# Kernel tuning notes

Measured on AMD Instinct MI355X. Metric: run time of the kernel, lower is better.

## Reference

```python
import jax, jax.numpy as jnp
import numpy as np

N_HEADS = 16
HEAD_DIM = 64
N_EMBD = 1024
B, S = 2, 2048


def setup_inputs() -> dict:
    key = jax.random.key(0)
    k1, k2, k3 = jax.random.split(key, 3)
    x = jax.random.normal(k1, (B, S, N_EMBD), dtype=jnp.float32)
    W_attn = jax.random.normal(k2, (N_EMBD, 3 * N_EMBD), dtype=jnp.float32) * 0.02
    b_attn = jnp.zeros((3 * N_EMBD,), dtype=jnp.float32)
    W_proj = jax.random.normal(k3, (N_EMBD, N_EMBD), dtype=jnp.float32) * 0.02
    b_proj = jnp.zeros((N_EMBD,), dtype=jnp.float32)
    return {"x": x, "W_attn": W_attn, "b_attn": b_attn, "W_proj": W_proj, "b_proj": b_proj}


def reference(x, W_attn, b_attn, W_proj, b_proj):
    b, s, _ = x.shape
    qkv = x @ W_attn + b_attn  # (b, s, 3*n_embd)
    q, k, v = jnp.split(qkv, 3, axis=-1)
    # (b, s, n_embd) -> (b, h, s, d)
    def heads(t):
        return t.reshape(b, s, N_HEADS, HEAD_DIM).transpose(0, 2, 1, 3)
    q, k, v = heads(q), heads(k), heads(v)
    scale = 1.0 / jnp.sqrt(jnp.float32(HEAD_DIM))
    scores = jnp.einsum("bhqd,bhkd->bhqk", q, k) * scale
    causal = jnp.triu(jnp.full((s, s), -jnp.inf, dtype=scores.dtype), k=1)
    scores = scores + causal[None, None, :, :]
    attn = jax.nn.softmax(scores, axis=-1)
    out = jnp.einsum("bhqk,bhkd->bhqd", attn, v)  # (b, h, s, d)
    out = out.transpose(0, 2, 1, 3).reshape(b, s, N_EMBD)
    return out @ W_proj + b_proj
```

## Files before the change

kernel.cpp:

```cpp
#include <hip/hip_runtime.h>
#include <hip/hip_bf16.h>
#include <stdint.h>
#include <stddef.h>

typedef __bf16 bf16_t;
typedef __attribute__((ext_vector_type(8))) __bf16 bf16x8;
typedef __attribute__((ext_vector_type(4))) __bf16 bf16x4;
typedef __attribute__((ext_vector_type(4))) float f32x4;

#define MFMA_BF16(a, b, c) __builtin_amdgcn_mfma_f32_16x16x32_bf16((a), (b), (c), 0, 0, 0)

__global__ void detect_dtype(const unsigned short* __restrict__ x, int* __restrict__ flag) {
  __shared__ int cnt;
  if (threadIdx.x == 0) cnt = 0;
  __syncthreads();
  int local = 0;
  for (int i = threadIdx.x; i < 16384; i += 256) {
    const int e = (x[i] >> 7) & 0xFF;
    if (e >= 0x8D) local++;
  }
  atomicAdd(&cnt, local);
  __syncthreads();
  if (threadIdx.x == 0) *flag = (cnt > 16) ? 1 : 0;
}

__global__ void cvt_x(const float* __restrict__ in, bf16_t* __restrict__ out,
                      const int* __restrict__ flagp) {
  if (!*flagp) return;
  const size_t i = ((size_t)blockIdx.x * 256 + threadIdx.x) * 8;
  const float4 a = *(const float4*)(in + i), b = *(const float4*)(in + i + 4);
  bf16x8 r;
  r[0] = (__bf16)a.x; r[1] = (__bf16)a.y; r[2] = (__bf16)a.z; r[3] = (__bf16)a.w;
  r[4] = (__bf16)b.x; r[5] = (__bf16)b.y; r[6] = (__bf16)b.z; r[7] = (__bf16)b.w;
  *(bf16x8*)(out + i) = r;
}

__global__ void transpose_any(const void* __restrict__ in, bf16_t* __restrict__ out,
                              int R, int C, const int* __restrict__ flagp) {
  const int isF32 = *flagp;
  __shared__ bf16_t tile[32][33];
  const int tx = threadIdx.x, ty = threadIdx.y;
  const int r0 = blockIdx.y * 32, c0 = blockIdx.x * 32;
#pragma unroll
  for (int i = 0; i < 4; ++i) {
    const size_t idx = (size_t)(r0 + ty + i * 8) * C + (c0 + tx);
    tile[ty + i * 8][tx] = isF32 ? (bf16_t)((const float*)in)[idx]
                                 : ((const bf16_t*)in)[idx];
  }
  __syncthreads();
#pragma unroll
  for (int i = 0; i < 4; ++i)
    out[(size_t)(c0 + ty + i * 8) * R + (r0 + tx)] = tile[tx][ty + i * 8];
}

#define GP 72
template <int MODE>
__global__ __launch_bounds__(256) void gemm_bt(const void* A0,
                        const bf16_t* __restrict__ xb,
                        const bf16_t* __restrict__ Bt,
                        const void* __restrict__ bias,
                        void* C,
                        bf16_t* __restrict__ Qs,
                        bf16_t* __restrict__ Kb,
                        bf16_t* __restrict__ dout_bf,
                        int M, int N, int K,
                        const int* __restrict__ flagp) {
  const int isF32 = *flagp;
  const bf16_t* A = (MODE == 1 && isF32) ? xb : (const bf16_t*)A0;
  bf16_t* Vt = dout_bf + (isF32 ? (size_t)4194304 : 0);

  __shared__ __align__(16) unsigned char pool[128 * GP * 2 * 2];
  bf16_t* As = (bf16_t*)pool;
  bf16_t* Bs = (bf16_t*)pool + 128 * GP;

  const int tid = threadIdx.x;
  const int w = tid >> 6, lane = tid & 63;
  const int quad = lane >> 4, l16 = lane & 15;
  const int wm = w >> 1, wn = w & 1;
  const int m0 = blockIdx.y * 128, n0 = blockIdx.x * 128;

  auto loadA = [&](int k0, int it) -> bf16x8 {
    const int g = it * 256 + tid;
    const int row = g >> 3, col = (g & 7) * 8;
    const int m = m0 + row;
    if (MODE == 2) {
      const size_t aoff =
          ((size_t)((m >> 11) * 16 + (k0 >> 6)) * 2048 + (m & 2047)) * 64 + col;
      return *(const bf16x8*)(A + aoff);
    }
    return *(const bf16x8*)(A + (size_t)m * K + (k0 + col));
  };
  auto loadB = [&](int k0, int it) -> bf16x8 {
    const int g = it * 256 + tid;
    const int row = g >> 3, col = (g & 7) * 8;
    return *(const bf16x8*)(Bt + (size_t)(n0 + row) * K + (k0 + col));
  };

  f32x4 acc[4][4];
#pragma unroll
  for (int i = 0; i < 4; ++i)
#pragma unroll
    for (int j = 0; j < 4; ++j) acc[i][j] = f32x4{0.f, 0.f, 0.f, 0.f};

  auto stage = [&](bf16x8* va, bf16x8* vb) {
#pragma unroll
    for (int it = 0; it < 4; ++it) {
      const int g = it * 256 + tid;
      const int row = g >> 3, col = (g & 7) * 8;
      *(bf16x8*)&As[row * GP + col] = va[it];
      *(bf16x8*)&Bs[row * GP + col] = vb[it];
    }
  };
  auto compute = [&]() {
#pragma unroll
    for (int kc = 0; kc < 2; ++kc) {
      bf16x8 af[4], bfr[4];
#pragma unroll
      for (int i = 0; i < 4; ++i)
        af[i] = *(const bf16x8*)&As[(wm * 64 + i * 16 + l16) * GP + kc * 32 + quad * 8];
#pragma unroll
      for (int j = 0; j < 4; ++j)
        bfr[j] = *(const bf16x8*)&Bs[(wn * 64 + j * 16 + l16) * GP + kc * 32 + quad * 8];
      __builtin_amdgcn_s_setprio(1);
#pragma unroll
      for (int i = 0; i < 4; ++i)
#pragma unroll
        for (int j = 0; j < 4; ++j) acc[i][j] = MFMA_BF16(af[i], bfr[j], acc[i][j]);
      __builtin_amdgcn_s_setprio(0);
    }
  };

  bf16x8 va0[4], vb0[4], va1[4], vb1[4];
#pragma unroll
  for (int it = 0; it < 4; ++it) { va0[it] = loadA(0, it);  vb0[it] = loadB(0, it); }
#pragma unroll
  for (int it = 0; it < 4; ++it) { va1[it] = loadA(64, it); vb1[it] = loadB(64, it); }

  for (int k0 = 0; k0 < K; k0 += 128) {
    __syncthreads();
    stage(va0, vb0);
    __syncthreads();
    if (k0 + 128 < K) {
#pragma unroll
      for (int it = 0; it < 4; ++it) { va0[it] = loadA(k0 + 128, it); vb0[it] = loadB(k0 + 128, it); }
    }
    compute();
    __syncthreads();
    stage(va1, vb1);
    __syncthreads();
    if (k0 + 192 < K) {
#pragma unroll
      for (int it = 0; it < 4; ++it) { va1[it] = loadA(k0 + 192, it); vb1[it] = loadB(k0 + 192, it); }
    }
    compute();
  }

  if (MODE == 1 && n0 >= 2048) {
    bf16_t* tp = (bf16_t*)pool;
    __syncthreads();
#pragma unroll
    for (int j = 0; j < 4; ++j) {
      const int n_l = wn * 64 + j * 16 + l16;
      const int n = n0 + n_l;
      const float bj = isF32 ? ((const float*)bias)[n] : (float)((const bf16_t*)bias)[n];
#pragma unroll
      for (int i = 0; i < 4; ++i) {
#pragma unroll
        for (int r = 0; r < 4; ++r) {
          const int m_l = wm * 64 + i * 16 + quad * 4 + r;
          tp[n_l * 136 + m_l] = (bf16_t)(acc[i][j][r] + bj);
        }
      }
    }
    __syncthreads();
    const int b = m0 >> 11, s0 = m0 & 2047;
#pragma unroll
    for (int seg = 0; seg < 8; ++seg) {
      const int idx = seg * 256 + tid;
      const int n_l = idx >> 4, ms = (idx & 15) * 8;
      const bf16x8 v8 = *(const bf16x8*)&tp[n_l * 136 + ms];
      const int e = (n0 + n_l) & 1023, h = e >> 6, d = e & 63;
      *(bf16x8*)(Vt + ((size_t)(b * 16 + h) * 64 + d) * 2048 + s0 + ms) = v8;
    }
    return;
  }

  if (MODE == 1) {
    bf16_t* tp = (bf16_t*)pool;
    __syncthreads();
    const bool isQ = (n0 < 1024);
    const float sc = isQ ? 0.18033688011f : 1.0f;
#pragma unroll
    for (int j = 0; j < 4; ++j) {
      const int n_l = wn * 64 + j * 16 + l16;
      const int n = n0 + n_l;
      const float bj = isF32 ? ((const float*)bias)[n] : (float)((const bf16_t*)bias)[n];
#pragma unroll
      for (int i = 0; i < 4; ++i) {
#pragma unroll
        for (int r = 0; r < 4; ++r) {
          const int m_l = wm * 64 + i * 16 + quad * 4 + r;
          tp[m_l * 136 + n_l] = (bf16_t)((acc[i][j][r] + bj) * sc);
        }
      }
    }
    __syncthreads();
    bf16_t* dst = isQ ? Qs : Kb;
#pragma unroll
    for (int seg = 0; seg < 8; ++seg) {
      const int idx = seg * 256 + tid;
      const int m_l = idx >> 4, ns = (idx & 15) * 8;
      const bf16x8 v8 = *(const bf16x8*)&tp[m_l * 136 + ns];
      const int m = m0 + m_l;
      const int e = (n0 + ns) & 1023, h = e >> 6, d = e & 63;
      const int bb = m >> 11, s = m & 2047;
      *(bf16x8*)(dst + (((size_t)(bb * 16 + h) * 2048 + s) * 64 + d)) = v8;
    }
    return;
  }

#pragma unroll
  for (int j = 0; j < 4; ++j) {
    const int n = n0 + wn * 64 + j * 16 + l16;
    const float bj = isF32 ? ((const float*)bias)[n] : (float)((const bf16_t*)bias)[n];
#pragma unroll
    for (int i = 0; i < 4; ++i) {
      const int mbase = m0 + wm * 64 + i * 16 + quad * 4;
#pragma unroll
      for (int r = 0; r < 4; ++r) {
        const int m = mbase + r;
        const float v = acc[i][j][r] + bj;
        if (isF32) ((float*)C)[(size_t)m * N + n] = v;
        else       ((bf16_t*)C)[(size_t)m * N + n] = (bf16_t)v;
      }
    }
  }
}

#define AP 72
#define PSP 72
__global__ __launch_bounds__(256, 5) void attn_kernel(bf16_t* QO,
                                                      const bf16_t* __restrict__ Kb,
                                                      const bf16_t* __restrict__ dout_bf,
                                                      const int* __restrict__ flagp) {
  const int isF32 = *flagp;
  const bf16_t* Vt = dout_bf + (isF32 ? (size_t)4194304 : 0);

  __shared__ __align__(16) bf16_t Ks[64 * AP];
  __shared__ __align__(16) bf16_t Vs[64 * AP];
  __shared__ __align__(16) bf16_t Ps[4][16 * PSP];

  const int bid = blockIdx.x;
  const int g = bid >> 5, bh = bid & 31;
  const int qt = (g < 16) ? (31 - g) : (g - 16);

  const int tid = threadIdx.x, w = tid >> 6, lane = tid & 63;
  const int quad = lane >> 4, l16 = lane & 15;

  bf16_t* Q = QO + (size_t)bh * 2048 * 64;
  const bf16_t* K = Kb + (size_t)bh * 2048 * 64;
  const bf16_t* V = Vt + (size_t)bh * 64 * 2048;

  const int qrow = qt * 64 + w * 16;
  const int nkt = qt + 1;

  bf16x8 qf[2];
#pragma unroll
  for (int kk = 0; kk < 2; ++kk)
    qf[kk] = *(const bf16x8*)(Q + (size_t)(qrow + l16) * 64 + kk * 32 + quad * 8);

  f32x4 oacc[4];
  float lsum = 0.f;
#pragma unroll
  for (int jd = 0; jd < 4; ++jd) oacc[jd] = f32x4{0.f, 0.f, 0.f, 0.f};

  const int srow8 = lane >> 3;
  const int scol8 = (lane & 7) * 8;

  auto loadK = [&](int kt, int it) -> bf16x8 {
    const int row = (w + it * 4) * 8 + srow8;
    return *(const bf16x8*)(K + (size_t)(kt * 64 + row) * 64 + scol8);
  };
  auto loadV = [&](int kt, int it) -> bf16x8 {
    const int row = (w + it * 4) * 8 + srow8;
    return *(const bf16x8*)(V + (size_t)row * 2048 + kt * 64 + scol8);
  };

  bf16x8 kv[2], vv[2];
#pragma unroll
  for (int it = 0; it < 2; ++it) { kv[it] = loadK(0, it); vv[it] = loadV(0, it); }

  for (int kt = 0; kt < nkt; ++kt) {
    __syncthreads();
#pragma unroll
    for (int it = 0; it < 2; ++it) {
      const int row = (w + it * 4) * 8 + srow8;
      *(bf16x8*)&Ks[row * AP + scol8] = kv[it];
      *(bf16x8*)&Vs[row * AP + scol8] = vv[it];
    }
    __syncthreads();

    if (kt + 1 < nkt) {
#pragma unroll
      for (int it = 0; it < 2; ++it) { kv[it] = loadK(kt + 1, it); vv[it] = loadV(kt + 1, it); }
    }

    const int kbase = kt * 64;
    f32x4 s[4];
    __builtin_amdgcn_s_setprio(1);
#pragma unroll
    for (int j = 0; j < 4; ++j) {
      const bf16x8 kf0 = *(const bf16x8*)&Ks[(j * 16 + l16) * AP + quad * 8];
      const bf16x8 kf1 = *(const bf16x8*)&Ks[(j * 16 + l16) * AP + 32 + quad * 8];
      f32x4 z = f32x4{0.f, 0.f, 0.f, 0.f};
      z = MFMA_BF16(kf0, qf[0], z);
      s[j] = MFMA_BF16(kf1, qf[1], z);
    }
    __builtin_amdgcn_s_setprio(0);

    if (kbase + 63 > qrow) {
      const int qg = qrow + l16;
#pragma unroll
      for (int j = 0; j < 4; ++j) {
        const int key = kbase + j * 16 + quad * 4;
#pragma unroll
        for (int r = 0; r < 4; ++r)
          if (key + r > qg) s[j][r] = -1e30f;
      }
    }

#pragma unroll
    for (int j = 0; j < 4; ++j) {
      bf16x4 pk;
#pragma unroll
      for (int r = 0; r < 4; ++r) {
        const float p = exp2f(s[j][r]);
        lsum += p;
        pk[r] = (__bf16)p;
      }
      *(bf16x4*)&Ps[w][l16 * PSP + j * 16 + quad * 4] = pk;
    }

    __builtin_amdgcn_s_setprio(1);
#pragma unroll
    for (int kk = 0; kk < 2; ++kk) {
      const bf16x8 pf = *(const bf16x8*)&Ps[w][l16 * PSP + kk * 32 + quad * 8];
#pragma unroll
      for (int jd = 0; jd < 4; ++jd) {
        const bf16x8 vf = *(const bf16x8*)&Vs[(jd * 16 + l16) * AP + kk * 32 + quad * 8];
        oacc[jd] = MFMA_BF16(pf, vf, oacc[jd]);
      }
    }
    __builtin_amdgcn_s_setprio(0);
  }

  lsum += __shfl_xor(lsum, 16);
  lsum += __shfl_xor(lsum, 32);

#pragma unroll
  for (int r = 0; r < 4; ++r) {
    const float lr = fmaxf(__shfl(lsum, quad * 4 + r, 16), 1e-30f);
    const int q = qrow + quad * 4 + r;
#pragma unroll
    for (int jd = 0; jd < 4; ++jd) {
      const int d = jd * 16 + l16;
      Q[(size_t)q * 64 + d] = (bf16_t)(oacc[jd][r] / lr);
    }
  }
}

extern "C" void kernel_launch(void* const* d_in, const int* in_sizes, int n_in,
                              void* d_out, int out_size, void* d_ws, size_t ws_size,
                              hipStream_t stream) {
  const void* x      = d_in[0];
  const void* W_attn = d_in[1];
  const void* b_attn = d_in[2];
  const void* W_proj = d_in[3];
  const void* b_proj = d_in[4];

  char* ws = (char*)d_ws;
  size_t off = 0;
  auto alloc = [&](size_t bytes) {
    char* p = ws + off;
    off += (bytes + 255) & ~(size_t)255;
    return p;
  };
  int*    flag = (int*)alloc(256);
  bf16_t* Qs   = (bf16_t*)alloc((size_t)32 * 2048 * 64 * 2);
  bf16_t* Kb   = (bf16_t*)alloc((size_t)32 * 2048 * 64 * 2);
  bf16_t* Wat  = (bf16_t*)alloc((size_t)3072 * 1024 * 2);
  bf16_t* Wpt  = (bf16_t*)alloc((size_t)1024 * 1024 * 2);
  bf16_t* dout_bf = (bf16_t*)d_out;

  detect_dtype<<<1, 256, 0, stream>>>((const unsigned short*)x, flag);

  cvt_x<<<2048, 256, 0, stream>>>((const float*)x, dout_bf, flag);

  transpose_any<<<dim3(3072 / 32, 1024 / 32), dim3(32, 8), 0, stream>>>(W_attn, Wat, 1024, 3072, flag);
  transpose_any<<<dim3(1024 / 32, 1024 / 32), dim3(32, 8), 0, stream>>>(W_proj, Wpt, 1024, 1024, flag);

  gemm_bt<1><<<dim3(3072 / 128, 4096 / 128), 256, 0, stream>>>(
      x, dout_bf, Wat, b_attn, nullptr, Qs, Kb, dout_bf, 4096, 3072, 1024, flag);

  attn_kernel<<<dim3(1024), 256, 0, stream>>>(Qs, Kb, dout_bf, flag);

  gemm_bt<2><<<dim3(1024 / 128, 4096 / 128), 256, 0, stream>>>(
      Qs, nullptr, Wpt, b_proj, d_out, nullptr, nullptr, dout_bf, 4096, 1024, 1024, flag);
}
```

Baseline: 199.5 us.

## Fuse prep kernels into one launch, single-buffer GEMM loop, drop setprio

Merges dtype detection, x conversion and both weight transposes into one prep kernel, where every block redoes a smaller dtype check on the first 4096 halfwords, which saves three launches. The GEMM main loop goes from two register-prefetch buffers over 128-wide K steps to a single buffer over 64-wide steps, which cuts register pressure but adds a barrier pair per step. The s_setprio hints are removed from both the GEMM and the attention kernels. The detection threshold changes, and each block repeating the check adds a little redundant work.

```diff
diff --git a/kernel.cpp b/kernel.cpp
--- a/kernel.cpp
+++ b/kernel.cpp
@@ -10,42 +10,66 @@
 
 #define MFMA_BF16(a, b, c) __builtin_amdgcn_mfma_f32_16x16x32_bf16((a), (b), (c), 0, 0, 0)
 
-__global__ void detect_dtype(const unsigned short* __restrict__ x, int* __restrict__ flag) {
-  __shared__ int cnt;
-  if (threadIdx.x == 0) cnt = 0;
+__global__ __launch_bounds__(256) void prep(const void* __restrict__ x,
+                                            const void* __restrict__ Wa,
+                                            const void* __restrict__ Wp,
+                                            bf16_t* __restrict__ xb,
+                                            bf16_t* __restrict__ Wat,
+                                            bf16_t* __restrict__ Wpt,
+                                            int* __restrict__ flag) {
+  __shared__ int dcnt;
+  __shared__ bf16_t tile[32][33];
+
+  const int tid = threadIdx.x;
+  if (tid == 0) dcnt = 0;
   __syncthreads();
-  int local = 0;
-  for (int i = threadIdx.x; i < 16384; i += 256) {
-    const int e = (x[i] >> 7) & 0xFF;
-    if (e >= 0x8D) local++;
-  }
-  atomicAdd(&cnt, local);
+  {
+    const unsigned short* p = (const unsigned short*)x + tid * 16;
+    int local = 0;
+#pragma unroll
+    for (int i = 0; i < 16; ++i) {
+      const int e = (p[i] >> 7) & 0xFF;
+      if (e >= 0x8D) local++;
+    }
+    if (local) atomicAdd(&dcnt, local);
+  }
   __syncthreads();
-  if (threadIdx.x == 0) *flag = (cnt > 16) ? 1 : 0;
-}
-
-__global__ void cvt_x(const float* __restrict__ in, bf16_t* __restrict__ out,
-                      const int* __restrict__ flagp) {
-  if (!*flagp) return;
-  const size_t i = ((size_t)blockIdx.x * 256 + threadIdx.x) * 8;
-  const float4 a = *(const float4*)(in + i), b = *(const float4*)(in + i + 4);
-  bf16x8 r;
-  r[0] = (__bf16)a.x; r[1] = (__bf16)a.y; r[2] = (__bf16)a.z; r[3] = (__bf16)a.w;
-  r[4] = (__bf16)b.x; r[5] = (__bf16)b.y; r[6] = (__bf16)b.z; r[7] = (__bf16)b.w;
-  *(bf16x8*)(out + i) = r;
-}
-
-__global__ void transpose_any(const void* __restrict__ in, bf16_t* __restrict__ out,
-                              int R, int C, const int* __restrict__ flagp) {
-  const int isF32 = *flagp;
-  __shared__ bf16_t tile[32][33];
-  const int tx = threadIdx.x, ty = threadIdx.y;
-  const int r0 = blockIdx.y * 32, c0 = blockIdx.x * 32;
+  const int isF32 = (dcnt > 4) ? 1 : 0;
+
+  const int b = blockIdx.x;
+  if (b == 0 && tid == 0) *flag = isF32;
+
+  if (b < 2048) {
+    if (!isF32) return;
+    const size_t i = ((size_t)b * 256 + tid) * 8;
+    const float4 a0 = *(const float4*)((const float*)x + i);
+    const float4 a1 = *(const float4*)((const float*)x + i + 4);
+    bf16x8 r;
+    r[0] = (__bf16)a0.x; r[1] = (__bf16)a0.y; r[2] = (__bf16)a0.z; r[3] = (__bf16)a0.w;
+    r[4] = (__bf16)a1.x; r[5] = (__bf16)a1.y; r[6] = (__bf16)a1.z; r[7] = (__bf16)a1.w;
+    *(bf16x8*)(xb + i) = r;
+    return;
+  }
+
+  const void* in;
+  bf16_t* out;
+  int R, C, bx, by;
+  if (b < 5120) {
+    const int idx = b - 2048;
+    in = Wa; out = Wat; R = 1024; C = 3072;
+    bx = idx % 96; by = idx / 96;
+  } else {
+    const int idx = b - 5120;
+    in = Wp; out = Wpt; R = 1024; C = 1024;
+    bx = idx & 31; by = idx >> 5;
+  }
+  const int tx = tid & 31, ty = tid >> 5;
+  const int r0 = by * 32, c0 = bx * 32;
 #pragma unroll
   for (int i = 0; i < 4; ++i) {
-    const size_t idx = (size_t)(r0 + ty + i * 8) * C + (c0 + tx);
-    tile[ty + i * 8][tx] = isF32 ? (bf16_t)((const float*)in)[idx]
-                                 : ((const bf16_t*)in)[idx];
+    const size_t idx2 = (size_t)(r0 + ty + i * 8) * C + (c0 + tx);
+    tile[ty + i * 8][tx] = isF32 ? (bf16_t)((const float*)in)[idx2]
+                                 : ((const bf16_t*)in)[idx2];
   }
   __syncthreads();
 #pragma unroll
@@ -102,7 +126,12 @@
 #pragma unroll
     for (int j = 0; j < 4; ++j) acc[i][j] = f32x4{0.f, 0.f, 0.f, 0.f};
 
-  auto stage = [&](bf16x8* va, bf16x8* vb) {
+  bf16x8 va[4], vb[4];
+#pragma unroll
+  for (int it = 0; it < 4; ++it) { va[it] = loadA(0, it); vb[it] = loadB(0, it); }
+
+  for (int k0 = 0; k0 < K; k0 += 64) {
+    __syncthreads();
 #pragma unroll
     for (int it = 0; it < 4; ++it) {
       const int g = it * 256 + tid;
@@ -110,8 +139,13 @@
       *(bf16x8*)&As[row * GP + col] = va[it];
       *(bf16x8*)&Bs[row * GP + col] = vb[it];
     }
-  };
-  auto compute = [&]() {
+    __syncthreads();
+
+    if (k0 + 64 < K) {
+#pragma unroll
+      for (int it = 0; it < 4; ++it) { va[it] = loadA(k0 + 64, it); vb[it] = loadB(k0 + 64, it); }
+    }
+
 #pragma unroll
     for (int kc = 0; kc < 2; ++kc) {
       bf16x8 af[4], bfr[4];
@@ -121,38 +155,11 @@
 #pragma unroll
       for (int j = 0; j < 4; ++j)
         bfr[j] = *(const bf16x8*)&Bs[(wn * 64 + j * 16 + l16) * GP + kc * 32 + quad * 8];
-      __builtin_amdgcn_s_setprio(1);
 #pragma unroll
       for (int i = 0; i < 4; ++i)
 #pragma unroll
         for (int j = 0; j < 4; ++j) acc[i][j] = MFMA_BF16(af[i], bfr[j], acc[i][j]);
-      __builtin_amdgcn_s_setprio(0);
-    }
-  };
-
-  bf16x8 va0[4], vb0[4], va1[4], vb1[4];
-#pragma unroll
-  for (int it = 0; it < 4; ++it) { va0[it] = loadA(0, it);  vb0[it] = loadB(0, it); }
-#pragma unroll
-  for (int it = 0; it < 4; ++it) { va1[it] = loadA(64, it); vb1[it] = loadB(64, it); }
-
-  for (int k0 = 0; k0 < K; k0 += 128) {
-    __syncthreads();
-    stage(va0, vb0);
-    __syncthreads();
-    if (k0 + 128 < K) {
-#pragma unroll
-      for (int it = 0; it < 4; ++it) { va0[it] = loadA(k0 + 128, it); vb0[it] = loadB(k0 + 128, it); }
-    }
-    compute();
-    __syncthreads();
-    stage(va1, vb1);
-    __syncthreads();
-    if (k0 + 192 < K) {
-#pragma unroll
-      for (int it = 0; it < 4; ++it) { va1[it] = loadA(k0 + 192, it); vb1[it] = loadB(k0 + 192, it); }
-    }
-    compute();
+    }
   }
 
   if (MODE == 1 && n0 >= 2048) {
@@ -307,7 +314,6 @@
 
     const int kbase = kt * 64;
     f32x4 s[4];
-    __builtin_amdgcn_s_setprio(1);
 #pragma unroll
     for (int j = 0; j < 4; ++j) {
       const bf16x8 kf0 = *(const bf16x8*)&Ks[(j * 16 + l16) * AP + quad * 8];
@@ -316,7 +322,6 @@
       z = MFMA_BF16(kf0, qf[0], z);
       s[j] = MFMA_BF16(kf1, qf[1], z);
     }
-    __builtin_amdgcn_s_setprio(0);
 
     if (kbase + 63 > qrow) {
       const int qg = qrow + l16;
@@ -341,7 +346,6 @@
       *(bf16x4*)&Ps[w][l16 * PSP + j * 16 + quad * 4] = pk;
     }
 
-    __builtin_amdgcn_s_setprio(1);
 #pragma unroll
     for (int kk = 0; kk < 2; ++kk) {
       const bf16x8 pf = *(const bf16x8*)&Ps[w][l16 * PSP + kk * 32 + quad * 8];
@@ -351,7 +355,6 @@
         oacc[jd] = MFMA_BF16(pf, vf, oacc[jd]);
       }
     }
-    __builtin_amdgcn_s_setprio(0);
   }
 
   lsum += __shfl_xor(lsum, 16);
@@ -392,12 +395,7 @@
   bf16_t* Wpt  = (bf16_t*)alloc((size_t)1024 * 1024 * 2);
   bf16_t* dout_bf = (bf16_t*)d_out;
 
-  detect_dtype<<<1, 256, 0, stream>>>((const unsigned short*)x, flag);
-
-  cvt_x<<<2048, 256, 0, stream>>>((const float*)x, dout_bf, flag);
-
-  transpose_any<<<dim3(3072 / 32, 1024 / 32), dim3(32, 8), 0, stream>>>(W_attn, Wat, 1024, 3072, flag);
-  transpose_any<<<dim3(1024 / 32, 1024 / 32), dim3(32, 8), 0, stream>>>(W_proj, Wpt, 1024, 1024, flag);
+  prep<<<dim3(6144), 256, 0, stream>>>(x, W_attn, W_proj, dout_bf, Wat, Wpt, flag);
 
   gemm_bt<1><<<dim3(3072 / 128, 4096 / 128), 256, 0, stream>>>(
       x, dout_bf, Wat, b_attn, nullptr, Qs, Kb, dout_bf, 4096, 3072, 1024, flag);
```

Measured after the change: 189.7 us. 1.05x faster.
